# Kernel optimization log

Hardware: AMD Instinct MI355X
Metric: run time of the kernel (lower is better)

The kernel has to match this reference:

```python
import jax, jax.numpy as jnp
import numpy as np

COLOR_LIST = np.array([[0, 0, 0], [0.5, 0.5, 1], [0, 1, 1], [0.5, 1, 0], [1, 0, 1],
                       [1, 0.5, 0.5], [1, 0, 0.5], [0.5, 1, 0.5], [1, 1, 0],
                       [0.5, 0.5, 0.5], [1, 1, 1]], dtype=np.float32)
IMG_WEIGHT = 1.0
ATTRI, SQE, H, W = 6, 14, 128, 128


def _check_colors(gen_T):
    # gen_T: (N, 14, 4, H, W). Vectorized version of per-sample/per-slot check_color.
    rgb = gen_T[:, :, :3]      # (N,14,3,H,W)
    alpha = gen_T[:, :, -1:]   # (N,14,1,H,W), broadcasts over the 3 rgb channels
    c0 = jnp.sum(((rgb > 0) & (rgb < 0.2) & (alpha > 0.8)).astype(jnp.int32), axis=(-1, -2))
    c1 = jnp.sum(((rgb > 0.4) & (rgb < 0.6)).astype(jnp.int32), axis=(-1, -2))
    c2 = jnp.sum((rgb > 0.8).astype(jnp.int32), axis=(-1, -2))
    vals = jnp.where((c2 > c1) & (c2 > c0), 1.0,
                     jnp.where(c1 > c0, 0.5, 0.0)).astype(jnp.float32)  # (N,14,3)
    colors = jnp.asarray(COLOR_LIST)  # (11,3)
    member = jnp.any(jnp.all(vals[:, :, None, :] == colors[None, None], axis=-1), axis=-1)  # (N,14)
    out = jnp.where(member[..., None], vals, 0.0)
    # torch builds Type_list from fresh tensors -> detached from the graph
    return jax.lax.stop_gradient(out)


def _norm_global(x):
    # Faithful to normalize_per_batch: GLOBAL min/max over the whole tensor.
    mx = x.max()
    mn = x.min()
    return (x - mn) / (mx - mn)


def setup_inputs() -> dict:
    key = jax.random.key(0)
    k1, k2 = jax.random.split(key)
    GT = jax.random.uniform(k1, (8, 4, H, W), dtype=jnp.float32)
    Pred = jax.random.uniform(k2, (8, ATTRI, SQE, 4, H, W), dtype=jnp.float32)
    return {"GT": GT, "Pred": Pred}


def reference(GT, Pred):
    N = GT.shape[0]
    GT_norm = (GT[:, :-1] + 1.0) / 2.0                      # (N,3,H,W)
    gen = _norm_global(Pred).reshape(N, ATTRI, SQE, 4, H, W)
    gen_T = gen[:, 0]                                       # (N,14,4,H,W)
    gen_L = jnp.sum(gen[:, 2, :, :-1], axis=1)              # (N,3,H,W)
    gen_A = jnp.sum(gen[:, 3, :, :-1], axis=1)
    gen_R = gen[:, 4, :, :-1]                               # (N,14,3,H,W)
    gen_W = jnp.sum(gen[:, 5, :, :-1], axis=1)

    type_list = _check_colors(gen_T)                        # (N,14,3)

    t = 10.0
    region_soft = (jax.nn.sigmoid((gen_R[:, :, 0] - 0.9) * t)
                   * jax.nn.sigmoid((gen_R[:, :, 1] - 0.9) * t)
                   * jax.nn.sigmoid((gen_R[:, :, 2] - 0.9) * t))  # (N,14,H,W)

    weighted = region_soft[:, :, None] * type_list[:, :, :, None, None]  # (N,14,3,H,W)
    region_contrib = _norm_global(weighted.sum(axis=1))     # (N,3,H,W)

    composite = jnp.clip(region_contrib + gen_L + gen_A + gen_W, 0.0, 1.0)
    loss = jnp.mean((composite - GT_norm) ** 2)
    return loss * IMG_WEIGHT
```

## Files before the change

kernel.cpp:

```cpp
#include <hip/hip_runtime.h>
#include <math.h>

#define ATTRI 6
#define SQE   14
#define HWPX  16384
#define NB    8
#define S_C   HWPX
#define S_S   (4 * HWPX)
#define S_A   (SQE * 4 * HWPX)
#define S_N   (ATTRI * SQE * 4 * HWPX)
#define NPRED (NB * S_N)
#define NOUT  (NB * 3 * HWPX)

#define WS_MM     0
#define WS_COUNTS 16
#define WS_LAW    4096
#define WS_WSUM   (4096 + NOUT * 4)
#define WS_PART   (WS_WSUM + NOUT * 4)

__device__ __forceinline__ unsigned fkey(float f) {
    unsigned u = __float_as_uint(f);
    return (u & 0x80000000u) ? ~u : (u | 0x80000000u);
}
__device__ __forceinline__ float fdec(unsigned k) {
    unsigned u = (k & 0x80000000u) ? (k & 0x7FFFFFFFu) : ~k;
    return __uint_as_float(u);
}
__device__ __forceinline__ float sigm(float x) { return 1.0f / (1.0f + expf(-x)); }

__global__ void k_init(unsigned* mm, int* counts) {
    int t = threadIdx.x;
    if (t == 0) { mm[0] = 0xFF800000u; mm[2] = 0xFF800000u; }
    if (t == 1) { mm[1] = 0x007FFFFFu; mm[3] = 0x007FFFFFu; }
    for (int i = t; i < NB * SQE * 9; i += blockDim.x) counts[i] = 0;
}

__global__ __launch_bounds__(256) void k_minmax(const float4* __restrict__ p, unsigned* mm) {
    float lmin = INFINITY, lmax = -INFINITY;
    int stride = gridDim.x * blockDim.x;
    for (int i = blockIdx.x * blockDim.x + threadIdx.x; i < NPRED / 4; i += stride) {
        float4 v = p[i];
        lmin = fminf(fminf(lmin, fminf(v.x, v.y)), fminf(v.z, v.w));
        lmax = fmaxf(fmaxf(lmax, fmaxf(v.x, v.y)), fmaxf(v.z, v.w));
    }
#pragma unroll
    for (int o = 32; o; o >>= 1) {
        lmin = fminf(lmin, __shfl_down(lmin, o));
        lmax = fmaxf(lmax, __shfl_down(lmax, o));
    }
    __shared__ float smin[4], smax[4];
    int wid = threadIdx.x >> 6, lane = threadIdx.x & 63;
    if (lane == 0) { smin[wid] = lmin; smax[wid] = lmax; }
    __syncthreads();
    if (threadIdx.x == 0) {
        float bmin = fminf(fminf(smin[0], smin[1]), fminf(smin[2], smin[3]));
        float bmax = fmaxf(fmaxf(smax[0], smax[1]), fmaxf(smax[2], smax[3]));
        atomicMin(&mm[0], fkey(bmin));
        atomicMax(&mm[1], fkey(bmax));
    }
}

__global__ __launch_bounds__(256) void k_counts_law(const float* __restrict__ pred,
                                                    const unsigned* __restrict__ mm,
                                                    int* counts, float* __restrict__ law) {
    float mn = fdec(mm[0]);
    float d  = fdec(mm[1]) - mn;
    int b = blockIdx.x;
    if (b < 896) {
        int pair = b >> 3, slice = b & 7;
        int n = pair / SQE, s = pair % SQE;
        const float* base = pred + (size_t)n * S_N + (size_t)s * S_S;
        int cnt[9];
#pragma unroll
        for (int j = 0; j < 9; j++) cnt[j] = 0;
        for (int k = 0; k < 8; k++) {
            int p = slice * 2048 + k * 256 + threadIdx.x;
            float a = (base[3 * S_C + p] - mn) / d;
            bool av = a > 0.8f;
#pragma unroll
            for (int ch = 0; ch < 3; ch++) {
                float g = (base[ch * S_C + p] - mn) / d;
                cnt[ch * 3 + 0] += (g > 0.0f && g < 0.2f && av) ? 1 : 0;
                cnt[ch * 3 + 1] += (g > 0.4f && g < 0.6f) ? 1 : 0;
                cnt[ch * 3 + 2] += (g > 0.8f) ? 1 : 0;
            }
        }
#pragma unroll
        for (int o = 32; o; o >>= 1) {
#pragma unroll
            for (int j = 0; j < 9; j++) cnt[j] += __shfl_down(cnt[j], o);
        }
        __shared__ int sc[4][9];
        int wid = threadIdx.x >> 6, lane = threadIdx.x & 63;
        if (lane == 0) {
#pragma unroll
            for (int j = 0; j < 9; j++) sc[wid][j] = cnt[j];
        }
        __syncthreads();
        if (threadIdx.x < 9) {
            int tot = sc[0][threadIdx.x] + sc[1][threadIdx.x] + sc[2][threadIdx.x] + sc[3][threadIdx.x];
            atomicAdd(&counts[(n * SQE + s) * 9 + threadIdx.x], tot);
        }
    } else {
        int idx = (b - 896) * 256 + threadIdx.x;
        int hw = idx & (HWPX - 1);
        int nc = idx >> 14;
        int n = nc / 3, c = nc - 3 * (nc / 3);
        const float* pn = pred + (size_t)n * S_N + (size_t)c * S_C + hw;
        float sL = 0.f, sA = 0.f, sW = 0.f;
        for (int s = 0; s < SQE; s++) {
            size_t o = (size_t)s * S_S;
            sL += (pn[2 * (size_t)S_A + o] - mn) / d;
            sA += (pn[3 * (size_t)S_A + o] - mn) / d;
            sW += (pn[5 * (size_t)S_A + o] - mn) / d;
        }
        law[idx] = (sL + sA) + sW;
    }
}

__global__ __launch_bounds__(256) void k_wsum(const float* __restrict__ pred,
                                              unsigned* mm, const int* __restrict__ counts,
                                              float* __restrict__ wsum) {
    __shared__ float tl[SQE][3];
    int tid = threadIdx.x;
    int n = blockIdx.x >> 6;
    if (tid < SQE * 3) {
        int s = tid / 3, ch = tid - 3 * (tid / 3);
        const int* cc = counts + (n * SQE + s) * 9 + ch * 3;
        int c0 = cc[0], c1 = cc[1], c2 = cc[2];
        tl[s][ch] = (c2 > c1 && c2 > c0) ? 1.0f : ((c1 > c0) ? 0.5f : 0.0f);
    }
    __syncthreads();
    if (tid < SQE) {
        int code = (int)(tl[tid][0] * 2.0f) * 9 + (int)(tl[tid][1] * 2.0f) * 3 + (int)(tl[tid][2] * 2.0f);
        if (!((0x0559E101u >> code) & 1u)) { tl[tid][0] = 0.f; tl[tid][1] = 0.f; tl[tid][2] = 0.f; }
    }
    __syncthreads();

    float mn = fdec(mm[0]);
    float d  = fdec(mm[1]) - mn;
    int idx = blockIdx.x * 256 + tid;
    int hw = idx & (HWPX - 1);
    const float* pr = pred + (size_t)n * S_N + 4 * (size_t)S_A + hw;
    float a0 = 0.f, a1 = 0.f, a2 = 0.f;
    for (int s = 0; s < SQE; s++) {
        const float* ps = pr + (size_t)s * S_S;
        float g0 = (ps[0] - mn) / d;
        float g1 = (ps[S_C] - mn) / d;
        float g2 = (ps[2 * S_C] - mn) / d;
        float r = sigm((g0 - 0.9f) * 10.0f) * sigm((g1 - 0.9f) * 10.0f) * sigm((g2 - 0.9f) * 10.0f);
        a0 += r * tl[s][0];
        a1 += r * tl[s][1];
        a2 += r * tl[s][2];
    }
    wsum[(n * 3 + 0) * HWPX + hw] = a0;
    wsum[(n * 3 + 1) * HWPX + hw] = a1;
    wsum[(n * 3 + 2) * HWPX + hw] = a2;

    float lmin = fminf(a0, fminf(a1, a2));
    float lmax = fmaxf(a0, fmaxf(a1, a2));
#pragma unroll
    for (int o = 32; o; o >>= 1) {
        lmin = fminf(lmin, __shfl_down(lmin, o));
        lmax = fmaxf(lmax, __shfl_down(lmax, o));
    }
    __shared__ float smin[4], smax[4];
    int wid = tid >> 6, lane = tid & 63;
    if (lane == 0) { smin[wid] = lmin; smax[wid] = lmax; }
    __syncthreads();
    if (tid == 0) {
        float bmin = fminf(fminf(smin[0], smin[1]), fminf(smin[2], smin[3]));
        float bmax = fmaxf(fmaxf(smax[0], smax[1]), fmaxf(smax[2], smax[3]));
        atomicMin(&mm[2], fkey(bmin));
        atomicMax(&mm[3], fkey(bmax));
    }
}

__global__ __launch_bounds__(512) void k_loss(const float* __restrict__ gt,
                                              const unsigned* __restrict__ mm,
                                              const float* __restrict__ law,
                                              const float* __restrict__ wsum,
                                              float* __restrict__ part) {
    float mn2 = fdec(mm[2]);
    float d2  = fdec(mm[3]) - mn2;
    int idx = blockIdx.x * 512 + threadIdx.x;
    int hw = idx & (HWPX - 1);
    int nc = idx >> 14;
    int n = nc / 3, c = nc - 3 * (nc / 3);
    float gtn = (gt[((size_t)(n * 4 + c)) * HWPX + hw] + 1.0f) * 0.5f;
    float rc = (wsum[idx] - mn2) / d2;
    float comp = rc + law[idx];
    comp = fminf(fmaxf(comp, 0.0f), 1.0f);
    float diff = comp - gtn;
    float se = diff * diff;

    __shared__ float sdata[512];
    sdata[threadIdx.x] = se;
    __syncthreads();
#pragma unroll
    for (int s = 256; s > 0; s >>= 1) {
        if (threadIdx.x < s) sdata[threadIdx.x] += sdata[threadIdx.x + s];
        __syncthreads();
    }
    if (threadIdx.x == 0) part[blockIdx.x] = sdata[0];
}

__global__ __launch_bounds__(256) void k_final(const float* __restrict__ part, float* __restrict__ out) {
    __shared__ float sdata[256];
    float v = part[threadIdx.x] + part[threadIdx.x + 256] + part[threadIdx.x + 512];
    sdata[threadIdx.x] = v;
    __syncthreads();
#pragma unroll
    for (int s = 128; s > 0; s >>= 1) {
        if (threadIdx.x < s) sdata[threadIdx.x] += sdata[threadIdx.x + s];
        __syncthreads();
    }
    if (threadIdx.x == 0) out[0] = sdata[0] / (float)NOUT;
}

extern "C" void kernel_launch(void* const* d_in, const int* in_sizes, int n_in,
                              void* d_out, int out_size, void* d_ws, size_t ws_size,
                              hipStream_t stream) {
    const float* GT   = (const float*)d_in[0];
    const float* Pred = (const float*)d_in[1];
    float* out = (float*)d_out;
    char* ws = (char*)d_ws;
    unsigned* mm = (unsigned*)(ws + WS_MM);
    int* counts  = (int*)(ws + WS_COUNTS);
    float* law   = (float*)(ws + WS_LAW);
    float* wsum  = (float*)(ws + WS_WSUM);
    float* part  = (float*)(ws + WS_PART);

    k_init<<<1, 256, 0, stream>>>(mm, counts);
    k_minmax<<<1536, 256, 0, stream>>>((const float4*)Pred, mm);
    k_counts_law<<<896 + NOUT / 256, 256, 0, stream>>>(Pred, mm, counts, law);
    k_wsum<<<NB * HWPX / 256, 256, 0, stream>>>(Pred, mm, counts, wsum);
    k_loss<<<NOUT / 512, 512, 0, stream>>>(GT, mm, law, wsum, part);
    k_final<<<1, 256, 0, stream>>>(part, out);
}
```

Before: 318.8 us.

## Fuse raw L/A/W sums into global min-max pass and drop extra kernels

The global min/max pass now also sums the raw L, A and W planes with float4 loads, and normalization is applied later algebraically as (sum - 42*mn)/d. This removes a separate full read of those planes after the min/max pass. The remaining Pred planes are covered by per-plane min/max blocks. The counts kernel is vectorized with float4, the init kernel becomes a memset, and the final reduction is folded into the loss kernel through a last-block atomic counter. The wsum loop skips slots whose type color is zero. The algebraic normalization can change rounding slightly, and the plane coverage of the min/max pass depends on hand-written index mapping.

Result: faster. 310.3 us (-2.7%).

```diff
diff --git a/kernel.cpp b/kernel.cpp
--- a/kernel.cpp
+++ b/kernel.cpp
@@ -13,7 +13,8 @@
 #define NOUT  (NB * 3 * HWPX)
 
 #define WS_MM     0
-#define WS_COUNTS 16
+#define WS_CTR    16
+#define WS_COUNTS 32
 #define WS_LAW    4096
 #define WS_WSUM   (4096 + NOUT * 4)
 #define WS_PART   (WS_WSUM + NOUT * 4)
@@ -28,93 +29,119 @@
 }
 __device__ __forceinline__ float sigm(float x) { return 1.0f / (1.0f + expf(-x)); }
 
-__global__ void k_init(unsigned* mm, int* counts) {
-    int t = threadIdx.x;
-    if (t == 0) { mm[0] = 0xFF800000u; mm[2] = 0xFF800000u; }
-    if (t == 1) { mm[1] = 0x007FFFFFu; mm[3] = 0x007FFFFFu; }
-    for (int i = t; i < NB * SQE * 9; i += blockDim.x) counts[i] = 0;
-}
-
-__global__ __launch_bounds__(256) void k_minmax(const float4* __restrict__ p, unsigned* mm) {
-    float lmin = INFINITY, lmax = -INFINITY;
-    int stride = gridDim.x * blockDim.x;
-    for (int i = blockIdx.x * blockDim.x + threadIdx.x; i < NPRED / 4; i += stride) {
-        float4 v = p[i];
-        lmin = fminf(fminf(lmin, fminf(v.x, v.y)), fminf(v.z, v.w));
-        lmax = fmaxf(fmaxf(lmax, fmaxf(v.x, v.y)), fmaxf(v.z, v.w));
-    }
+__device__ __forceinline__ void blk_minmax_atomic(float mnl, float mxl, unsigned* mm, int mmOff) {
 #pragma unroll
     for (int o = 32; o; o >>= 1) {
-        lmin = fminf(lmin, __shfl_down(lmin, o));
-        lmax = fmaxf(lmax, __shfl_down(lmax, o));
-    }
-    __shared__ float smin[4], smax[4];
+        mnl = fminf(mnl, __shfl_down(mnl, o));
+        mxl = fmaxf(mxl, __shfl_down(mxl, o));
+    }
+    __shared__ float smn[4], smx[4];
     int wid = threadIdx.x >> 6, lane = threadIdx.x & 63;
-    if (lane == 0) { smin[wid] = lmin; smax[wid] = lmax; }
+    if (lane == 0) { smn[wid] = mnl; smx[wid] = mxl; }
     __syncthreads();
     if (threadIdx.x == 0) {
-        float bmin = fminf(fminf(smin[0], smin[1]), fminf(smin[2], smin[3]));
-        float bmax = fmaxf(fmaxf(smax[0], smax[1]), fmaxf(smax[2], smax[3]));
-        atomicMin(&mm[0], fkey(bmin));
-        atomicMax(&mm[1], fkey(bmax));
-    }
-}
-
-__global__ __launch_bounds__(256) void k_counts_law(const float* __restrict__ pred,
-                                                    const unsigned* __restrict__ mm,
-                                                    int* counts, float* __restrict__ law) {
-    float mn = fdec(mm[0]);
+        float bmn = fminf(fminf(smn[0], smn[1]), fminf(smn[2], smn[3]));
+        float bmx = fmaxf(fmaxf(smx[0], smx[1]), fmaxf(smx[2], smx[3]));
+        atomicMax(&mm[mmOff + 0], ~fkey(bmn));
+        atomicMax(&mm[mmOff + 1], fkey(bmx));
+    }
+}
+
+__global__ __launch_bounds__(256) void k_p1(const float* __restrict__ pred, unsigned* mm,
+                                            float4* __restrict__ slaw) {
+    float mnl = INFINITY, mxl = -INFINITY;
+    int b = blockIdx.x, t = threadIdx.x;
+    if (b < 384) {
+        int idx = b * 256 + t;
+        int hw4 = idx & 4095;
+        int nc = idx >> 12;
+        int n = nc / 3, c = nc - 3 * (nc / 3);
+        const float4* p = (const float4*)(pred + (size_t)n * S_N + (size_t)c * S_C) + hw4;
+        float4 s = make_float4(0.f, 0.f, 0.f, 0.f);
+        const int attrs[3] = {2, 3, 5};
+#pragma unroll
+        for (int ai = 0; ai < 3; ai++) {
+            const float4* pa = p + (size_t)attrs[ai] * (S_A / 4);
+#pragma unroll
+            for (int ss = 0; ss < SQE; ss++) {
+                float4 v = pa[(size_t)ss * (S_S / 4)];
+                s.x += v.x; s.y += v.y; s.z += v.z; s.w += v.w;
+                mnl = fminf(mnl, fminf(fminf(v.x, v.y), fminf(v.z, v.w)));
+                mxl = fmaxf(mxl, fmaxf(fmaxf(v.x, v.y), fmaxf(v.z, v.w)));
+            }
+        }
+        slaw[idx] = s;
+    } else {
+        int bb = b - 384;
+        int n = bb / 210, pi = bb - 210 * n;
+        int plane;
+        if (pi < 112)      plane = pi;
+        else if (pi < 126) plane = 112 + (pi - 112) * 4 + 3;
+        else if (pi < 140) plane = 168 + (pi - 126) * 4 + 3;
+        else if (pi < 196) plane = 224 + (pi - 140);
+        else               plane = 280 + (pi - 196) * 4 + 3;
+        const float4* p = (const float4*)(pred + (size_t)n * S_N + (size_t)plane * HWPX);
+#pragma unroll 4
+        for (int k = 0; k < 16; k++) {
+            float4 v = p[k * 256 + t];
+            mnl = fminf(mnl, fminf(fminf(v.x, v.y), fminf(v.z, v.w)));
+            mxl = fmaxf(mxl, fmaxf(fmaxf(v.x, v.y), fmaxf(v.z, v.w)));
+        }
+    }
+    blk_minmax_atomic(mnl, mxl, mm, 0);
+}
+
+__global__ __launch_bounds__(256) void k_counts(const float* __restrict__ pred,
+                                                const unsigned* __restrict__ mm,
+                                                int* __restrict__ counts) {
+    float mn = fdec(~mm[0]);
     float d  = fdec(mm[1]) - mn;
     int b = blockIdx.x;
-    if (b < 896) {
-        int pair = b >> 3, slice = b & 7;
-        int n = pair / SQE, s = pair % SQE;
-        const float* base = pred + (size_t)n * S_N + (size_t)s * S_S;
-        int cnt[9];
-#pragma unroll
-        for (int j = 0; j < 9; j++) cnt[j] = 0;
-        for (int k = 0; k < 8; k++) {
-            int p = slice * 2048 + k * 256 + threadIdx.x;
-            float a = (base[3 * S_C + p] - mn) / d;
+    int pair = b >> 3, slice = b & 7;
+    int n = pair / SQE, s = pair - SQE * (pair / SQE);
+    const float4* base = (const float4*)(pred + (size_t)n * S_N + (size_t)s * S_S);
+    int cnt[9];
+#pragma unroll
+    for (int j = 0; j < 9; j++) cnt[j] = 0;
+#pragma unroll
+    for (int k = 0; k < 2; k++) {
+        int p = slice * 512 + k * 256 + threadIdx.x;
+        float4 va = base[3 * 4096 + p];
+        float4 v0 = base[p];
+        float4 v1 = base[4096 + p];
+        float4 v2 = base[2 * 4096 + p];
+        const float ax[4] = {va.x, va.y, va.z, va.w};
+        const float cx[3][4] = {{v0.x, v0.y, v0.z, v0.w},
+                                {v1.x, v1.y, v1.z, v1.w},
+                                {v2.x, v2.y, v2.z, v2.w}};
+#pragma unroll
+        for (int e = 0; e < 4; e++) {
+            float a = (ax[e] - mn) / d;
             bool av = a > 0.8f;
 #pragma unroll
             for (int ch = 0; ch < 3; ch++) {
-                float g = (base[ch * S_C + p] - mn) / d;
+                float g = (cx[ch][e] - mn) / d;
                 cnt[ch * 3 + 0] += (g > 0.0f && g < 0.2f && av) ? 1 : 0;
                 cnt[ch * 3 + 1] += (g > 0.4f && g < 0.6f) ? 1 : 0;
                 cnt[ch * 3 + 2] += (g > 0.8f) ? 1 : 0;
             }
         }
-#pragma unroll
-        for (int o = 32; o; o >>= 1) {
-#pragma unroll
-            for (int j = 0; j < 9; j++) cnt[j] += __shfl_down(cnt[j], o);
-        }
-        __shared__ int sc[4][9];
-        int wid = threadIdx.x >> 6, lane = threadIdx.x & 63;
-        if (lane == 0) {
-#pragma unroll
-            for (int j = 0; j < 9; j++) sc[wid][j] = cnt[j];
-        }
-        __syncthreads();
-        if (threadIdx.x < 9) {
-            int tot = sc[0][threadIdx.x] + sc[1][threadIdx.x] + sc[2][threadIdx.x] + sc[3][threadIdx.x];
-            atomicAdd(&counts[(n * SQE + s) * 9 + threadIdx.x], tot);
-        }
-    } else {
-        int idx = (b - 896) * 256 + threadIdx.x;
-        int hw = idx & (HWPX - 1);
-        int nc = idx >> 14;
-        int n = nc / 3, c = nc - 3 * (nc / 3);
-        const float* pn = pred + (size_t)n * S_N + (size_t)c * S_C + hw;
-        float sL = 0.f, sA = 0.f, sW = 0.f;
-        for (int s = 0; s < SQE; s++) {
-            size_t o = (size_t)s * S_S;
-            sL += (pn[2 * (size_t)S_A + o] - mn) / d;
-            sA += (pn[3 * (size_t)S_A + o] - mn) / d;
-            sW += (pn[5 * (size_t)S_A + o] - mn) / d;
-        }
-        law[idx] = (sL + sA) + sW;
+    }
+#pragma unroll
+    for (int o = 32; o; o >>= 1) {
+#pragma unroll
+        for (int j = 0; j < 9; j++) cnt[j] += __shfl_down(cnt[j], o);
+    }
+    __shared__ int sc[4][9];
+    int wid = threadIdx.x >> 6, lane = threadIdx.x & 63;
+    if (lane == 0) {
+#pragma unroll
+        for (int j = 0; j < 9; j++) sc[wid][j] = cnt[j];
+    }
+    __syncthreads();
+    if (threadIdx.x < 9) {
+        int tot = sc[0][threadIdx.x] + sc[1][threadIdx.x] + sc[2][threadIdx.x] + sc[3][threadIdx.x];
+        atomicAdd(&counts[(n * SQE + s) * 9 + threadIdx.x], tot);
     }
 }
 
@@ -137,60 +164,53 @@
     }
     __syncthreads();
 
-    float mn = fdec(mm[0]);
+    float mn = fdec(~mm[0]);
     float d  = fdec(mm[1]) - mn;
     int idx = blockIdx.x * 256 + tid;
     int hw = idx & (HWPX - 1);
     const float* pr = pred + (size_t)n * S_N + 4 * (size_t)S_A + hw;
     float a0 = 0.f, a1 = 0.f, a2 = 0.f;
     for (int s = 0; s < SQE; s++) {
-        const float* ps = pr + (size_t)s * S_S;
-        float g0 = (ps[0] - mn) / d;
-        float g1 = (ps[S_C] - mn) / d;
-        float g2 = (ps[2 * S_C] - mn) / d;
-        float r = sigm((g0 - 0.9f) * 10.0f) * sigm((g1 - 0.9f) * 10.0f) * sigm((g2 - 0.9f) * 10.0f);
-        a0 += r * tl[s][0];
-        a1 += r * tl[s][1];
-        a2 += r * tl[s][2];
+        float t0 = tl[s][0], t1 = tl[s][1], t2 = tl[s][2];
+        if (t0 + t1 + t2 != 0.0f) {
+            const float* ps = pr + (size_t)s * S_S;
+            float g0 = (ps[0] - mn) / d;
+            float g1 = (ps[S_C] - mn) / d;
+            float g2 = (ps[2 * S_C] - mn) / d;
+            float r = sigm((g0 - 0.9f) * 10.0f) * sigm((g1 - 0.9f) * 10.0f) * sigm((g2 - 0.9f) * 10.0f);
+            a0 += r * t0;
+            a1 += r * t1;
+            a2 += r * t2;
+        }
     }
     wsum[(n * 3 + 0) * HWPX + hw] = a0;
     wsum[(n * 3 + 1) * HWPX + hw] = a1;
     wsum[(n * 3 + 2) * HWPX + hw] = a2;
 
-    float lmin = fminf(a0, fminf(a1, a2));
-    float lmax = fmaxf(a0, fmaxf(a1, a2));
-#pragma unroll
-    for (int o = 32; o; o >>= 1) {
-        lmin = fminf(lmin, __shfl_down(lmin, o));
-        lmax = fmaxf(lmax, __shfl_down(lmax, o));
-    }
-    __shared__ float smin[4], smax[4];
-    int wid = tid >> 6, lane = tid & 63;
-    if (lane == 0) { smin[wid] = lmin; smax[wid] = lmax; }
-    __syncthreads();
-    if (tid == 0) {
-        float bmin = fminf(fminf(smin[0], smin[1]), fminf(smin[2], smin[3]));
-        float bmax = fmaxf(fmaxf(smax[0], smax[1]), fmaxf(smax[2], smax[3]));
-        atomicMin(&mm[2], fkey(bmin));
-        atomicMax(&mm[3], fkey(bmax));
-    }
+    float mnl = fminf(a0, fminf(a1, a2));
+    float mxl = fmaxf(a0, fmaxf(a1, a2));
+    blk_minmax_atomic(mnl, mxl, mm, 2);
 }
 
 __global__ __launch_bounds__(512) void k_loss(const float* __restrict__ gt,
                                               const unsigned* __restrict__ mm,
-                                              const float* __restrict__ law,
+                                              const float* __restrict__ slaw,
                                               const float* __restrict__ wsum,
-                                              float* __restrict__ part) {
-    float mn2 = fdec(mm[2]);
+                                              float* __restrict__ part,
+                                              unsigned* __restrict__ ctr,
+                                              float* __restrict__ out) {
+    float mn  = fdec(~mm[0]);
+    float d   = fdec(mm[1]) - mn;
+    float mn2 = fdec(~mm[2]);
     float d2  = fdec(mm[3]) - mn2;
     int idx = blockIdx.x * 512 + threadIdx.x;
     int hw = idx & (HWPX - 1);
     int nc = idx >> 14;
     int n = nc / 3, c = nc - 3 * (nc / 3);
     float gtn = (gt[((size_t)(n * 4 + c)) * HWPX + hw] + 1.0f) * 0.5f;
-    float rc = (wsum[idx] - mn2) / d2;
-    float comp = rc + law[idx];
-    comp = fminf(fmaxf(comp, 0.0f), 1.0f);
+    float law = (slaw[idx] - 42.0f * mn) / d;
+    float rc  = (wsum[idx] - mn2) / d2;
+    float comp = fminf(fmaxf(rc + law, 0.0f), 1.0f);
     float diff = comp - gtn;
     float se = diff * diff;
 
@@ -202,20 +222,26 @@
         if (threadIdx.x < s) sdata[threadIdx.x] += sdata[threadIdx.x + s];
         __syncthreads();
     }
-    if (threadIdx.x == 0) part[blockIdx.x] = sdata[0];
-}
-
-__global__ __launch_bounds__(256) void k_final(const float* __restrict__ part, float* __restrict__ out) {
-    __shared__ float sdata[256];
-    float v = part[threadIdx.x] + part[threadIdx.x + 256] + part[threadIdx.x + 512];
-    sdata[threadIdx.x] = v;
-    __syncthreads();
-#pragma unroll
-    for (int s = 128; s > 0; s >>= 1) {
-        if (threadIdx.x < s) sdata[threadIdx.x] += sdata[threadIdx.x + s];
+    __shared__ int isLast;
+    if (threadIdx.x == 0) {
+        part[blockIdx.x] = sdata[0];
+        __threadfence();
+        unsigned prev = atomicAdd(ctr, 1u);
+        isLast = (prev == 767u) ? 1 : 0;
+        if (isLast) __threadfence();
+    }
+    __syncthreads();
+    if (isLast) {
+        float v = part[threadIdx.x] + ((threadIdx.x < 256) ? part[threadIdx.x + 512] : 0.0f);
+        sdata[threadIdx.x] = v;
         __syncthreads();
-    }
-    if (threadIdx.x == 0) out[0] = sdata[0] / (float)NOUT;
+#pragma unroll
+        for (int s = 256; s > 0; s >>= 1) {
+            if (threadIdx.x < s) sdata[threadIdx.x] += sdata[threadIdx.x + s];
+            __syncthreads();
+        }
+        if (threadIdx.x == 0) out[0] = sdata[0] / (float)NOUT;
+    }
 }
 
 extern "C" void kernel_launch(void* const* d_in, const int* in_sizes, int n_in,
@@ -225,16 +251,16 @@
     const float* Pred = (const float*)d_in[1];
     float* out = (float*)d_out;
     char* ws = (char*)d_ws;
-    unsigned* mm = (unsigned*)(ws + WS_MM);
-    int* counts  = (int*)(ws + WS_COUNTS);
-    float* law   = (float*)(ws + WS_LAW);
-    float* wsum  = (float*)(ws + WS_WSUM);
-    float* part  = (float*)(ws + WS_PART);
-
-    k_init<<<1, 256, 0, stream>>>(mm, counts);
-    k_minmax<<<1536, 256, 0, stream>>>((const float4*)Pred, mm);
-    k_counts_law<<<896 + NOUT / 256, 256, 0, stream>>>(Pred, mm, counts, law);
+    unsigned* mm   = (unsigned*)(ws + WS_MM);
+    unsigned* ctr  = (unsigned*)(ws + WS_CTR);
+    int* counts    = (int*)(ws + WS_COUNTS);
+    float* slaw    = (float*)(ws + WS_LAW);
+    float* wsum    = (float*)(ws + WS_WSUM);
+    float* part    = (float*)(ws + WS_PART);
+
+    hipMemsetAsync(ws, 0, 4096, stream);
+    k_p1<<<384 + NB * 210, 256, 0, stream>>>(Pred, mm, (float4*)slaw);
+    k_counts<<<896, 256, 0, stream>>>(Pred, mm, counts);
     k_wsum<<<NB * HWPX / 256, 256, 0, stream>>>(Pred, mm, counts, wsum);
-    k_loss<<<NOUT / 512, 512, 0, stream>>>(GT, mm, law, wsum, part);
-    k_final<<<1, 256, 0, stream>>>(part, out);
-}
+    k_loss<<<NOUT / 512, 512, 0, stream>>>(GT, mm, slaw, wsum, part, ctr, out);
+}
```
